# Kernel optimization log

Measured on AMD Instinct MI355X. Metric: run time of the kernel, lower is better.

Reference implementation:

```python
import math
import jax, jax.numpy as jnp
import numpy as np

D = 1024      # d_model
FF = 4096     # d_ff
E = 8         # num_experts
K = 2         # num_selected (top-k)
R = 2         # lora_rank (hardcoded in ToyMoEClassifier)
ALPHA = 4.0   # lora_alpha (hardcoded)
SCALE = ALPHA / R
CF = 1.25     # capacity_factor
NCLS = 2      # head output classes


def setup_inputs() -> dict:
    key = jax.random.key(0)
    ks = jax.random.split(key, 11)
    B, S = 4, 2048
    x = jax.random.normal(ks[0], (B, S, D), jnp.float32)
    Wg = jax.random.normal(ks[1], (D, E), jnp.float32) * 0.02
    W1 = jax.random.normal(ks[2], (D, FF), jnp.float32) * 0.02
    W2 = jax.random.normal(ks[3], (FF, D), jnp.float32) * 0.02
    A1 = jax.random.normal(ks[4], (E, D, R), jnp.float32) * 0.02
    B1 = jax.random.normal(ks[5], (E, R, FF), jnp.float32) * 0.02
    A2 = jax.random.normal(ks[6], (E, FF, R), jnp.float32) * 0.02
    B2 = jax.random.normal(ks[7], (E, R, D), jnp.float32) * 0.02
    Wh = jax.random.normal(ks[8], (D, NCLS), jnp.float32) * 0.02
    bh = jnp.zeros((NCLS,), jnp.float32)
    return {"x": x, "Wg": Wg, "W1": W1, "W2": W2, "A1": A1, "B1": B1,
            "A2": A2, "B2": B2, "Wh": Wh, "bh": bh}


def _moe_lora(x, Wg, W1, W2, A1, B1, A2, B2):
    B, S, d = x.shape
    T = B * S
    tok = x.reshape(T, d)                                  # [T, d]
    logits = tok @ Wg                                      # [T, E]
    vals, idx = jax.lax.top_k(logits, K)                   # [T, K]
    gates = jax.nn.softmax(vals, axis=-1)                  # renormalize over selected

    C = int(math.ceil(CF * T * K / E))                     # expert capacity (static)

    # position within expert, slot-major priority (slot 0 tokens first)
    onehot = jax.nn.one_hot(idx, E, dtype=jnp.float32)     # [T, K, E]
    m = onehot.transpose(1, 0, 2).reshape(K * T, E)        # [K*T, E]
    pos = jnp.cumsum(m, axis=0) - m
    pos_in = jnp.sum(pos * m, axis=-1).astype(jnp.int32)   # [K*T]
    exp_flat = idx.T.reshape(K * T)                        # [K*T]
    keep = (pos_in < C)
    w = gates.T.reshape(K * T) * keep.astype(gates.dtype)  # combine weight
    slot_idx = exp_flat * C + jnp.minimum(pos_in, C - 1)   # flat [E*C] index

    # dispatch: scatter kept tokens into per-expert capacity buffers
    disp = jnp.zeros((E * C, d), tok.dtype)
    for s in range(K):  # K is tiny and static
        sl = slice(s * T, (s + 1) * T)
        disp = disp.at[slot_idx[sl]].add(tok * keep[sl][:, None].astype(tok.dtype))
    disp3 = disp.reshape(E, C, d)

    # per-expert LoRA FFN: base weights shared, low-rank adapters per expert
    h = jax.nn.gelu(jnp.einsum('ecd,df->ecf', disp3, W1)
                    + SCALE * jnp.einsum('ecr,erf->ecf',
                                         jnp.einsum('ecd,edr->ecr', disp3, A1), B1))
    y = (jnp.einsum('ecf,fd->ecd', h, W2)
         + SCALE * jnp.einsum('ecr,erd->ecd',
                              jnp.einsum('ecf,efr->ecr', h, A2), B2))
    y_flat = y.reshape(E * C, d)

    # combine: gather expert outputs back, weighted by gates (dropped tokens -> 0)
    out = jnp.zeros((T, d), x.dtype)
    for s in range(K):
        sl = slice(s * T, (s + 1) * T)
        out = out + y_flat[slot_idx[sl]] * w[sl][:, None]
    return out.reshape(B, S, d)


def reference(x, Wg, W1, W2, A1, B1, A2, B2, Wh, bh):
    out = _moe_lora(x, Wg, W1, W2, A1, B1, A2, B2)   # [B, S, D]
    pooled = out.mean(axis=1)                        # [B, D]
    return pooled @ Wh + bh                          # [B, NCLS]
```

## Files before the change

### kernel.cpp

```cpp
#include <hip/hip_runtime.h>
#include <hip/hip_bf16.h>
#include <cstdint>
#include <cstddef>

#define D_MODEL 1024
#define FF_DIM  4096
#define NEXP    8
#define TOK     8192
#define CAP     2560
#define ECAP    (NEXP*CAP)
#define LSCALE  2.0f
#define SA_BYTE 124
#define SB_BYTE 122

typedef __attribute__((ext_vector_type(8))) int   int32x8;
typedef __attribute__((ext_vector_type(4))) float f32x4;
typedef __attribute__((ext_vector_type(2))) float f32x2;

__device__ __forceinline__ void gload16(const void* g, void* l){
  __builtin_amdgcn_global_load_lds((const __attribute__((address_space(1))) void*)g,
                                   (__attribute__((address_space(3))) void*)l, 16, 0, 0);
}
__device__ __forceinline__ float gelu_tanh(float x){
  float u = 0.7978845608028654f * (x + 0.044715f * x * x * x);
  float e = __expf(2.0f * u);
  float t = 1.0f - 2.0f / (e + 1.0f);
  return 0.5f * x * (1.0f + t);
}

__global__ void qt_both(const float* __restrict__ W1, const float* __restrict__ W2,
                        uint8_t* __restrict__ W1q, uint8_t* __restrict__ W2q)
{
  __shared__ float tile[64][65];
  const float* src; uint8_t* dst; int srcld, dstld;
  if (blockIdx.z == 0){ src = W1; dst = W1q; srcld = FF_DIM; dstld = D_MODEL; }
  else                { src = W2; dst = W2q; srcld = D_MODEL; dstld = FF_DIM; }
  int a0 = blockIdx.x * 64;
  int b0 = blockIdx.y * 64;
  if (blockIdx.z == 1){ a0 = blockIdx.y * 64; b0 = blockIdx.x * 64; }
  int tid = threadIdx.x;
  int r  = tid >> 4;
  int c4 = (tid & 15) * 4;
#pragma unroll
  for (int i = 0; i < 4; i++){
    int al = r + i*16;
    float4 v = *(const float4*)(src + (size_t)(a0 + al) * srcld + b0 + c4);
    tile[al][c4+0] = v.x; tile[al][c4+1] = v.y; tile[al][c4+2] = v.z; tile[al][c4+3] = v.w;
  }
  __syncthreads();
#pragma unroll
  for (int i = 0; i < 4; i++){
    int bl = r + i*16;
    int b  = b0 + bl;
    int pk = __builtin_amdgcn_cvt_pk_fp8_f32(32.f*tile[c4+0][bl], 32.f*tile[c4+1][bl], 0, false);
    pk     = __builtin_amdgcn_cvt_pk_fp8_f32(32.f*tile[c4+2][bl], 32.f*tile[c4+3][bl], pk, true);
    *(int*)(dst + (size_t)b * dstld + a0 + c4) = pk;
  }
}

__global__ void gate_kernel(const float* __restrict__ x, const float* __restrict__ Wg,
                            int* __restrict__ exp_flat, float* __restrict__ g_flat,
                            float* __restrict__ pooled, float* __restrict__ wslot)
{
  int gid = blockIdx.x * 256 + threadIdx.x;
  if (gid < 4*D_MODEL) pooled[gid] = 0.f;
  else if (gid < 4*D_MODEL + ECAP) wslot[gid - 4*D_MODEL] = 0.f;
  int lane = threadIdx.x & 63;
  int wave = threadIdx.x >> 6;
  int t = blockIdx.x * 4 + wave;
  const float4* xv = (const float4*)(x + (size_t)t * D_MODEL);
  float acc[8];
#pragma unroll
  for (int e = 0; e < 8; e++) acc[e] = 0.f;
#pragma unroll
  for (int i = 0; i < 4; i++){
    int i4 = lane + i*64;
    float4 v = xv[i4];
#pragma unroll
    for (int k = 0; k < 4; k++){
      float xs = (&v.x)[k];
      const float4* wr = (const float4*)(Wg + (size_t)(i4*4 + k) * 8);
      float4 w0 = wr[0], w1 = wr[1];
      acc[0] += xs*w0.x; acc[1] += xs*w0.y; acc[2] += xs*w0.z; acc[3] += xs*w0.w;
      acc[4] += xs*w1.x; acc[5] += xs*w1.y; acc[6] += xs*w1.z; acc[7] += xs*w1.w;
    }
  }
#pragma unroll
  for (int off = 32; off > 0; off >>= 1){
#pragma unroll
    for (int e = 0; e < 8; e++) acc[e] += __shfl_down(acc[e], off);
  }
  if (lane == 0){
    float m0 = acc[0]; int e0 = 0;
#pragma unroll
    for (int e = 1; e < 8; e++) if (acc[e] > m0){ m0 = acc[e]; e0 = e; }
    float m1 = -3.4e38f; int e1 = 0;
#pragma unroll
    for (int e = 0; e < 8; e++) if (e != e0 && acc[e] > m1){ m1 = acc[e]; e1 = e; }
    float z = __expf(m1 - m0);
    float inv = 1.f / (1.f + z);
    exp_flat[t]       = e0;
    exp_flat[TOK + t] = e1;
    g_flat[t]         = inv;
    g_flat[TOK + t]   = z * inv;
  }
}

__global__ __launch_bounds__(1024) void route_all(const int* __restrict__ exp_flat,
                                                  const float* __restrict__ g_flat,
                                                  int* __restrict__ slotidx,
                                                  float* __restrict__ wcomb,
                                                  int* __restrict__ fillc)
{
  __shared__ uint8_t rnk[16384];
  __shared__ uint8_t eexp[16384];
  __shared__ int     cnt[256*8];
  __shared__ int     grpoff[64];
  int tid = threadIdx.x;
  int lane = tid & 63, wv = tid >> 6;
  unsigned long long ltmask = (1ull << lane) - 1ull;
  for (int c = wv; c < 256; c += 16){
    int j = c*64 + lane;
    int e = exp_flat[j];
    eexp[j] = (uint8_t)e;
    int r = 0, myc = 0;
#pragma unroll
    for (int q = 0; q < 8; q++){
      unsigned long long m = __ballot(e == q);
      if (e == q) r = __popcll(m & ltmask);
      if (lane == q) myc = __popcll(m);
    }
    rnk[j] = (uint8_t)r;
    if (lane < 8) cnt[c*8 + lane] = myc;
  }
  __syncthreads();
  if (wv == 0){
    int e = lane & 7, g = lane >> 3;
    int run = 0;
    for (int c = g*32; c < g*32 + 32; c++){
      int v = cnt[c*8 + e];
      cnt[c*8 + e] = run;
      run += v;
    }
    int offs = 0, tot = 0;
#pragma unroll
    for (int gg = 0; gg < 8; gg++){
      int v = __shfl(run, gg*8 + e);
      if (gg < g) offs += v;
      tot += v;
    }
    grpoff[lane] = offs;
    if (g == 0) fillc[e] = tot < CAP ? tot : CAP;
  }
  __syncthreads();
  for (int j = tid; j < 16384; j += 1024){
    int e = eexp[j];
    int c = j >> 6;
    int pos = cnt[c*8 + e] + grpoff[(c >> 5)*8 + e] + rnk[j];
    bool keep = pos < CAP;
    slotidx[j] = e*CAP + (keep ? pos : (CAP-1));
    wcomb[j]   = keep ? g_flat[j] : 0.f;
  }
}

__global__ void dispatch_kernel(const float* __restrict__ x, const int* __restrict__ slotidx,
                                const float* __restrict__ wcomb, uint8_t* __restrict__ dispA,
                                float* __restrict__ wslot, int* __restrict__ tbat,
                                const float* __restrict__ A1, float* __restrict__ U1)
{
  int j = blockIdx.x;
  float w = wcomb[j];
  if (w == 0.f) return;
  int t = j & (TOK - 1);
  int slot = slotidx[j];
  int e = slot / CAP;
  int i = threadIdx.x;
  const float4* src = (const float4*)(x + (size_t)t * D_MODEL);
  float4 a = src[2*i], b = src[2*i+1];
  int p0 = __builtin_amdgcn_cvt_pk_fp8_f32(8.f*a.x, 8.f*a.y, 0, false);
  p0     = __builtin_amdgcn_cvt_pk_fp8_f32(8.f*a.z, 8.f*a.w, p0, true);
  int p1 = __builtin_amdgcn_cvt_pk_fp8_f32(8.f*b.x, 8.f*b.y, 0, false);
  p1     = __builtin_amdgcn_cvt_pk_fp8_f32(8.f*b.z, 8.f*b.w, p1, true);
  int2 o; o.x = p0; o.y = p1;
  *(int2*)(dispA + (size_t)slot * D_MODEL + i*8) = o;
  const float2* Av = (const float2*)(A1 + (size_t)e * D_MODEL * 2);
  int d0 = i*8;
  float xs[8] = {a.x,a.y,a.z,a.w,b.x,b.y,b.z,b.w};
  float pa = 0.f, pb = 0.f;
#pragma unroll
  for (int k = 0; k < 8; k++){
    float2 w2 = Av[d0 + k];
    pa += xs[k]*w2.x; pb += xs[k]*w2.y;
  }
#pragma unroll
  for (int off = 32; off > 0; off >>= 1){
    pa += __shfl_down(pa, off);
    pb += __shfl_down(pb, off);
  }
  __shared__ float red[4];
  int lane = i & 63, wv = i >> 6;
  if (lane == 0){ red[wv*2] = pa; red[wv*2+1] = pb; }
  __syncthreads();
  if (i == 0){
    U1[slot*2+0] = red[0] + red[2];
    U1[slot*2+1] = red[1] + red[3];
    wslot[slot] = w; tbat[slot] = t >> 11;
  }
}

__global__ void lora_u(const uint8_t* __restrict__ X, const float* __restrict__ Aw,
                       float* __restrict__ U, int Kdim)
{
  int lane = threadIdx.x & 63;
  int wv   = threadIdx.x >> 6;
  int slot = blockIdx.x * 4 + wv;
  int e = slot / CAP;
  const int4*   row = (const int4*)(X + (size_t)slot * Kdim);
  const float2* Av  = (const float2*)(Aw + (size_t)e * Kdim * 2);
  float a0 = 0.f, a1 = 0.f;
  int n16 = Kdim >> 4;
  for (int i = lane; i < n16; i += 64){
    int4 v = row[i];
    int d = i * 16;
#pragma unroll
    for (int c = 0; c < 4; c++){
      int w = (&v.x)[c];
      f32x2 f01 = __builtin_amdgcn_cvt_pk_f32_fp8(w, false);
      f32x2 f23 = __builtin_amdgcn_cvt_pk_f32_fp8(w, true);
      int dd = d + c*4;
      float2 w0 = Av[dd], w1 = Av[dd+1], w2 = Av[dd+2], w3 = Av[dd+3];
      a0 += f01.x*w0.x + f01.y*w1.x + f23.x*w2.x + f23.y*w3.x;
      a1 += f01.x*w0.y + f01.y*w1.y + f23.x*w2.y + f23.y*w3.y;
    }
  }
#pragma unroll
  for (int off = 32; off > 0; off >>= 1){
    a0 += __shfl_down(a0, off);
    a1 += __shfl_down(a1, off);
  }
  if (lane == 0){ U[slot*2] = a0 * 0.125f; U[slot*2+1] = a1 * 0.125f; }
}

template<bool GELU, bool COMBINE>
__global__ __launch_bounds__(256) void gemm_mx(const uint8_t* __restrict__ A,
                                               const uint8_t* __restrict__ Bt,
                                               uint8_t* __restrict__ Cb,
                                               int K, int N, const int* __restrict__ fillc,
                                               const float* __restrict__ U,
                                               const float* __restrict__ Bl,
                                               const float* __restrict__ wslot,
                                               const int* __restrict__ tbat,
                                               float* __restrict__ pooled)
{
  int e = blockIdx.x / 20;
  if ((blockIdx.x % 20) * 128 >= fillc[e]) return;
  int row0 = blockIdx.x * 128;
  int col0 = blockIdx.y * 128;

  __shared__ __align__(16) uint8_t As[128*128];
  __shared__ __align__(16) uint8_t Bs[128*128];
  __shared__ float part[COMBINE ? 512 : 4];

  int tid  = threadIdx.x;
  int lane = tid & 63;
  int wave = tid >> 6;
  int wm = wave & 1, wn = wave >> 1;

  if (COMBINE){ part[tid] = 0.f; part[tid + 256] = 0.f; }

  int r8 = lane >> 3;
  int cs = (lane & 7) ^ r8;
  const uint8_t* gA = A  + (size_t)(row0 + wave*32 + r8) * K + cs*16;
  const uint8_t* gB = Bt + (size_t)(col0 + wave*32 + r8) * K + cs*16;
  uint8_t* lA = As + wave*32*128;
  uint8_t* lB = Bs + wave*32*128;

  int rb = lane & 15;
  int q  = lane >> 4;

  f32x4 acc[4][4];
#pragma unroll
  for (int i = 0; i < 4; i++)
#pragma unroll
    for (int j = 0; j < 4; j++)
      acc[i][j] = (f32x4){0.f, 0.f, 0.f, 0.f};

  for (int k0 = 0; k0 < K; k0 += 128){
    __syncthreads();
#pragma unroll
    for (int g = 0; g < 4; g++){
      gload16(gA + k0 + (size_t)g*8*K, lA + g*1024);
      gload16(gB + k0 + (size_t)g*8*K, lB + g*1024);
    }
    __syncthreads();
    int32x8 a[4], b[4];
#pragma unroll
    for (int mt = 0; mt < 4; mt++){
      int row = wm*64 + mt*16 + rb;
      const uint8_t* base = As + row*128;
      int sw = row & 7;
      int4 lo = *(const int4*)(base + (((2*q)  ^sw)*16));
      int4 hi = *(const int4*)(base + (((2*q+1)^sw)*16));
      int32x8 v; v[0]=lo.x; v[1]=lo.y; v[2]=lo.z; v[3]=lo.w;
                 v[4]=hi.x; v[5]=hi.y; v[6]=hi.z; v[7]=hi.w;
      a[mt] = v;
    }
#pragma unroll
    for (int nt = 0; nt < 4; nt++){
      int row = wn*64 + nt*16 + rb;
      const uint8_t* base = Bs + row*128;
      int sw = row & 7;
      int4 lo = *(const int4*)(base + (((2*q)  ^sw)*16));
      int4 hi = *(const int4*)(base + (((2*q+1)^sw)*16));
      int32x8 v; v[0]=lo.x; v[1]=lo.y; v[2]=lo.z; v[3]=lo.w;
                 v[4]=hi.x; v[5]=hi.y; v[6]=hi.z; v[7]=hi.w;
      b[nt] = v;
    }
#pragma unroll
    for (int mt = 0; mt < 4; mt++)
#pragma unroll
      for (int nt = 0; nt < 4; nt++)
        acc[mt][nt] = __builtin_amdgcn_mfma_scale_f32_16x16x128_f8f6f4(
            a[mt], b[nt], acc[mt][nt], 0, 0, 0, SA_BYTE, 0, SB_BYTE);
  }

  float b0c[4], b1c[4];
#pragma unroll
  for (int nt = 0; nt < 4; nt++){
    int col = col0 + wn*64 + rb + nt*16;
    b0c[nt] = Bl[(e*2+0)*N + col];
    b1c[nt] = Bl[(e*2+1)*N + col];
  }

#pragma unroll
  for (int mt = 0; mt < 4; mt++){
#pragma unroll
    for (int r = 0; r < 4; r++){
      int row = row0 + wm*64 + mt*16 + q*4 + r;
      float2 u = *(const float2*)(U + row*2);
      float wv = 0.f; int tb = 0;
      if (COMBINE){ wv = wslot[row]; tb = tbat[row]; }
      size_t base = (size_t)row * N + col0 + wn*64 + rb;
#pragma unroll
      for (int nt = 0; nt < 4; nt++){
        float v = acc[mt][nt][r] + LSCALE*(u.x*b0c[nt] + u.y*b1c[nt]);
        if (GELU){
          v = gelu_tanh(v);
          int pk = __builtin_amdgcn_cvt_pk_fp8_f32(8.f*v, 0.f, 0, false);
          Cb[base + nt*16] = (uint8_t)(pk & 0xFF);
        }
        if (COMBINE){
          if (wv != 0.f) atomicAdd(&part[tb*128 + wn*64 + rb + nt*16], wv*v);
        }
      }
    }
  }

  if (COMBINE){
    __syncthreads();
#pragma unroll
    for (int idx = tid; idx < 512; idx += 256){
      float pv = part[idx];
      if (pv != 0.f) atomicAdd(pooled + (size_t)(idx >> 7) * D_MODEL + col0 + (idx & 127), pv);
    }
  }
}

__global__ void head_kernel(const float* __restrict__ pooled, const float* __restrict__ Wh,
                            const float* __restrict__ bh, float* __restrict__ out)
{
  int lane = threadIdx.x & 63;
  int wave = threadIdx.x >> 6;
  int b = wave >> 1, c = wave & 1;
  float s = 0.f;
#pragma unroll
  for (int i = 0; i < 16; i++){
    int d = lane + i*64;
    s += pooled[(size_t)b * D_MODEL + d] * Wh[d*2 + c];
  }
#pragma unroll
  for (int off = 32; off > 0; off >>= 1) s += __shfl_down(s, off);
  if (lane == 0) out[b*2 + c] = s * (1.0f/2048.0f) + bh[c];
}

extern "C" void kernel_launch(void* const* d_in, const int* in_sizes, int n_in,
                              void* d_out, int out_size, void* d_ws, size_t ws_size,
                              hipStream_t stream)
{
  const float* x  = (const float*)d_in[0];
  const float* Wg = (const float*)d_in[1];
  const float* W1 = (const float*)d_in[2];
  const float* W2 = (const float*)d_in[3];
  const float* A1 = (const float*)d_in[4];
  const float* B1 = (const float*)d_in[5];
  const float* A2 = (const float*)d_in[6];
  const float* B2 = (const float*)d_in[7];
  const float* Wh = (const float*)d_in[8];
  const float* bh = (const float*)d_in[9];
  float* out = (float*)d_out;

  char* p = (char*)d_ws;
  auto alloc = [&](size_t bytes){
    char* r = p;
    p += (bytes + 255) & ~(size_t)255;
    return (void*)r;
  };
  uint8_t* W1q   = (uint8_t*)alloc((size_t)FF_DIM*D_MODEL);
  uint8_t* W2q   = (uint8_t*)alloc((size_t)D_MODEL*FF_DIM);
  uint8_t* dispA = (uint8_t*)alloc((size_t)ECAP*D_MODEL);
  uint8_t* H     = (uint8_t*)alloc((size_t)ECAP*FF_DIM);
  float* U1       = (float*)alloc((size_t)ECAP*2*4);
  float* U2       = (float*)alloc((size_t)ECAP*2*4);
  float* wslot    = (float*)alloc((size_t)ECAP*4);
  int*   tbat     = (int*)  alloc((size_t)ECAP*4);
  int*   exp_flat = (int*)  alloc((size_t)2*TOK*4);
  float* g_flat   = (float*)alloc((size_t)2*TOK*4);
  int*   slotidx  = (int*)  alloc((size_t)2*TOK*4);
  float* wcomb    = (float*)alloc((size_t)2*TOK*4);
  int*   fillc    = (int*)  alloc(256);
  float* pooled   = (float*)alloc((size_t)4*D_MODEL*4);

  qt_both<<<dim3(16,64,2), 256, 0, stream>>>(W1, W2, W1q, W2q);
  gate_kernel<<<2048, 256, 0, stream>>>(x, Wg, exp_flat, g_flat, pooled, wslot);
  route_all<<<1, 1024, 0, stream>>>(exp_flat, g_flat, slotidx, wcomb, fillc);
  dispatch_kernel<<<2*TOK, 128, 0, stream>>>(x, slotidx, wcomb, dispA, wslot, tbat, A1, U1);
  gemm_mx<true, false><<<dim3(160,32), 256, 0, stream>>>(dispA, W1q, H, D_MODEL, FF_DIM,
                                                         fillc, U1, B1, nullptr, nullptr, nullptr);
  lora_u<<<5120, 256, 0, stream>>>(H, A2, U2, FF_DIM);
  gemm_mx<false, true><<<dim3(160,8), 256, 0, stream>>>(H, W2q, nullptr, FF_DIM, D_MODEL,
                                                        fillc, U2, B2, wslot, tbat, pooled);
  head_kernel<<<1, 512, 0, stream>>>(pooled, Wh, bh, out);
}
```

Before: 580.5 us.

## Halve GEMM M-tile to 64 rows and fuse gate with weight quantization

The fp8 MFMA GEMMs now use 64x128 tiles instead of 128x128. This doubles the grid, reduces skipped-tile waste at expert fill boundaries, and with launch_bounds(256,4) allows higher occupancy. The cost is less reuse of the B tile per loaded A row. The gating and weight-quantization kernels are merged into one launch so their blocks run concurrently and one launch is saved.

```diff
diff --git a/kernel.cpp b/kernel.cpp
--- a/kernel.cpp
+++ b/kernel.cpp
@@ -28,81 +28,82 @@
   return 0.5f * x * (1.0f + t);
 }
 
-__global__ void qt_both(const float* __restrict__ W1, const float* __restrict__ W2,
-                        uint8_t* __restrict__ W1q, uint8_t* __restrict__ W2q)
+__global__ void prep_kernel(const float* __restrict__ x, const float* __restrict__ Wg,
+                            int* __restrict__ exp_flat, float* __restrict__ g_flat,
+                            float* __restrict__ pooled, float* __restrict__ wslot,
+                            const float* __restrict__ W1, const float* __restrict__ W2,
+                            uint8_t* __restrict__ W1q, uint8_t* __restrict__ W2q)
 {
   __shared__ float tile[64][65];
-  const float* src; uint8_t* dst; int srcld, dstld;
-  if (blockIdx.z == 0){ src = W1; dst = W1q; srcld = FF_DIM; dstld = D_MODEL; }
-  else                { src = W2; dst = W2q; srcld = D_MODEL; dstld = FF_DIM; }
-  int a0 = blockIdx.x * 64;
-  int b0 = blockIdx.y * 64;
-  if (blockIdx.z == 1){ a0 = blockIdx.y * 64; b0 = blockIdx.x * 64; }
+  int bx = blockIdx.x;
   int tid = threadIdx.x;
-  int r  = tid >> 4;
-  int c4 = (tid & 15) * 4;
-#pragma unroll
-  for (int i = 0; i < 4; i++){
-    int al = r + i*16;
-    float4 v = *(const float4*)(src + (size_t)(a0 + al) * srcld + b0 + c4);
-    tile[al][c4+0] = v.x; tile[al][c4+1] = v.y; tile[al][c4+2] = v.z; tile[al][c4+3] = v.w;
-  }
-  __syncthreads();
-#pragma unroll
-  for (int i = 0; i < 4; i++){
-    int bl = r + i*16;
-    int b  = b0 + bl;
-    int pk = __builtin_amdgcn_cvt_pk_fp8_f32(32.f*tile[c4+0][bl], 32.f*tile[c4+1][bl], 0, false);
-    pk     = __builtin_amdgcn_cvt_pk_fp8_f32(32.f*tile[c4+2][bl], 32.f*tile[c4+3][bl], pk, true);
-    *(int*)(dst + (size_t)b * dstld + a0 + c4) = pk;
-  }
-}
-
-__global__ void gate_kernel(const float* __restrict__ x, const float* __restrict__ Wg,
-                            int* __restrict__ exp_flat, float* __restrict__ g_flat,
-                            float* __restrict__ pooled, float* __restrict__ wslot)
-{
-  int gid = blockIdx.x * 256 + threadIdx.x;
-  if (gid < 4*D_MODEL) pooled[gid] = 0.f;
-  else if (gid < 4*D_MODEL + ECAP) wslot[gid - 4*D_MODEL] = 0.f;
-  int lane = threadIdx.x & 63;
-  int wave = threadIdx.x >> 6;
-  int t = blockIdx.x * 4 + wave;
-  const float4* xv = (const float4*)(x + (size_t)t * D_MODEL);
-  float acc[8];
-#pragma unroll
-  for (int e = 0; e < 8; e++) acc[e] = 0.f;
-#pragma unroll
-  for (int i = 0; i < 4; i++){
-    int i4 = lane + i*64;
-    float4 v = xv[i4];
-#pragma unroll
-    for (int k = 0; k < 4; k++){
-      float xs = (&v.x)[k];
-      const float4* wr = (const float4*)(Wg + (size_t)(i4*4 + k) * 8);
-      float4 w0 = wr[0], w1 = wr[1];
-      acc[0] += xs*w0.x; acc[1] += xs*w0.y; acc[2] += xs*w0.z; acc[3] += xs*w0.w;
-      acc[4] += xs*w1.x; acc[5] += xs*w1.y; acc[6] += xs*w1.z; acc[7] += xs*w1.w;
-    }
-  }
-#pragma unroll
-  for (int off = 32; off > 0; off >>= 1){
-#pragma unroll
-    for (int e = 0; e < 8; e++) acc[e] += __shfl_down(acc[e], off);
-  }
-  if (lane == 0){
-    float m0 = acc[0]; int e0 = 0;
-#pragma unroll
-    for (int e = 1; e < 8; e++) if (acc[e] > m0){ m0 = acc[e]; e0 = e; }
-    float m1 = -3.4e38f; int e1 = 0;
-#pragma unroll
-    for (int e = 0; e < 8; e++) if (e != e0 && acc[e] > m1){ m1 = acc[e]; e1 = e; }
-    float z = __expf(m1 - m0);
-    float inv = 1.f / (1.f + z);
-    exp_flat[t]       = e0;
-    exp_flat[TOK + t] = e1;
-    g_flat[t]         = inv;
-    g_flat[TOK + t]   = z * inv;
+  if (bx < 2048){
+    int gid = bx * 256 + tid;
+    if (gid < 4*D_MODEL) pooled[gid] = 0.f;
+    else if (gid < 4*D_MODEL + ECAP) wslot[gid - 4*D_MODEL] = 0.f;
+    int lane = tid & 63;
+    int wave = tid >> 6;
+    int t = bx * 4 + wave;
+    const float4* xv = (const float4*)(x + (size_t)t * D_MODEL);
+    float acc[8];
+#pragma unroll
+    for (int e = 0; e < 8; e++) acc[e] = 0.f;
+#pragma unroll
+    for (int i = 0; i < 4; i++){
+      int i4 = lane + i*64;
+      float4 v = xv[i4];
+#pragma unroll
+      for (int k = 0; k < 4; k++){
+        float xs = (&v.x)[k];
+        const float4* wr = (const float4*)(Wg + (size_t)(i4*4 + k) * 8);
+        float4 w0 = wr[0], w1 = wr[1];
+        acc[0] += xs*w0.x; acc[1] += xs*w0.y; acc[2] += xs*w0.z; acc[3] += xs*w0.w;
+        acc[4] += xs*w1.x; acc[5] += xs*w1.y; acc[6] += xs*w1.z; acc[7] += xs*w1.w;
+      }
+    }
+#pragma unroll
+    for (int off = 32; off > 0; off >>= 1){
+#pragma unroll
+      for (int e = 0; e < 8; e++) acc[e] += __shfl_down(acc[e], off);
+    }
+    if (lane == 0){
+      float m0 = acc[0]; int e0 = 0;
+#pragma unroll
+      for (int e = 1; e < 8; e++) if (acc[e] > m0){ m0 = acc[e]; e0 = e; }
+      float m1 = -3.4e38f; int e1 = 0;
+#pragma unroll
+      for (int e = 0; e < 8; e++) if (e != e0 && acc[e] > m1){ m1 = acc[e]; e1 = e; }
+      float z = __expf(m1 - m0);
+      float inv = 1.f / (1.f + z);
+      exp_flat[t]       = e0;
+      exp_flat[TOK + t] = e1;
+      g_flat[t]         = inv;
+      g_flat[TOK + t]   = z * inv;
+    }
+  } else {
+    int b = bx - 2048;
+    int z = b >> 10; b &= 1023;
+    int bxx = b & 15, byy = b >> 4;
+    const float* src; uint8_t* dst; int srcld, dstld, a0, b0;
+    if (z == 0){ src = W1; dst = W1q; srcld = FF_DIM; dstld = D_MODEL; a0 = bxx*64; b0 = byy*64; }
+    else       { src = W2; dst = W2q; srcld = D_MODEL; dstld = FF_DIM; a0 = byy*64; b0 = bxx*64; }
+    int r  = tid >> 4;
+    int c4 = (tid & 15) * 4;
+#pragma unroll
+    for (int i = 0; i < 4; i++){
+      int al = r + i*16;
+      float4 v = *(const float4*)(src + (size_t)(a0 + al) * srcld + b0 + c4);
+      tile[al][c4+0] = v.x; tile[al][c4+1] = v.y; tile[al][c4+2] = v.z; tile[al][c4+3] = v.w;
+    }
+    __syncthreads();
+#pragma unroll
+    for (int i = 0; i < 4; i++){
+      int bl = r + i*16;
+      int bb = b0 + bl;
+      int pk = __builtin_amdgcn_cvt_pk_fp8_f32(32.f*tile[c4+0][bl], 32.f*tile[c4+1][bl], 0, false);
+      pk     = __builtin_amdgcn_cvt_pk_fp8_f32(32.f*tile[c4+2][bl], 32.f*tile[c4+3][bl], pk, true);
+      *(int*)(dst + (size_t)bb * dstld + a0 + c4) = pk;
+    }
   }
 }
 
@@ -242,22 +243,22 @@
 }
 
 template<bool GELU, bool COMBINE>
-__global__ __launch_bounds__(256) void gemm_mx(const uint8_t* __restrict__ A,
-                                               const uint8_t* __restrict__ Bt,
-                                               uint8_t* __restrict__ Cb,
-                                               int K, int N, const int* __restrict__ fillc,
-                                               const float* __restrict__ U,
-                                               const float* __restrict__ Bl,
-                                               const float* __restrict__ wslot,
-                                               const int* __restrict__ tbat,
-                                               float* __restrict__ pooled)
-{
-  int e = blockIdx.x / 20;
-  if ((blockIdx.x % 20) * 128 >= fillc[e]) return;
-  int row0 = blockIdx.x * 128;
+__global__ __launch_bounds__(256, 4) void gemm_mx(const uint8_t* __restrict__ A,
+                                                  const uint8_t* __restrict__ Bt,
+                                                  uint8_t* __restrict__ Cb,
+                                                  int K, int N, const int* __restrict__ fillc,
+                                                  const float* __restrict__ U,
+                                                  const float* __restrict__ Bl,
+                                                  const float* __restrict__ wslot,
+                                                  const int* __restrict__ tbat,
+                                                  float* __restrict__ pooled)
+{
+  int e = blockIdx.x / 40;
+  if ((blockIdx.x % 40) * 64 >= fillc[e]) return;
+  int row0 = blockIdx.x * 64;
   int col0 = blockIdx.y * 128;
 
-  __shared__ __align__(16) uint8_t As[128*128];
+  __shared__ __align__(16) uint8_t As[64*128];
   __shared__ __align__(16) uint8_t Bs[128*128];
   __shared__ float part[COMBINE ? 512 : 4];
 
@@ -270,17 +271,17 @@
 
   int r8 = lane >> 3;
   int cs = (lane & 7) ^ r8;
-  const uint8_t* gA = A  + (size_t)(row0 + wave*32 + r8) * K + cs*16;
+  const uint8_t* gA = A  + (size_t)(row0 + wave*16 + r8) * K + cs*16;
   const uint8_t* gB = Bt + (size_t)(col0 + wave*32 + r8) * K + cs*16;
-  uint8_t* lA = As + wave*32*128;
+  uint8_t* lA = As + wave*16*128;
   uint8_t* lB = Bs + wave*32*128;
 
   int rb = lane & 15;
   int q  = lane >> 4;
 
-  f32x4 acc[4][4];
-#pragma unroll
-  for (int i = 0; i < 4; i++)
+  f32x4 acc[2][4];
+#pragma unroll
+  for (int i = 0; i < 2; i++)
 #pragma unroll
     for (int j = 0; j < 4; j++)
       acc[i][j] = (f32x4){0.f, 0.f, 0.f, 0.f};
@@ -288,15 +289,16 @@
   for (int k0 = 0; k0 < K; k0 += 128){
     __syncthreads();
 #pragma unroll
-    for (int g = 0; g < 4; g++){
+    for (int g = 0; g < 2; g++)
       gload16(gA + k0 + (size_t)g*8*K, lA + g*1024);
+#pragma unroll
+    for (int g = 0; g < 4; g++)
       gload16(gB + k0 + (size_t)g*8*K, lB + g*1024);
-    }
     __syncthreads();
-    int32x8 a[4], b[4];
-#pragma unroll
-    for (int mt = 0; mt < 4; mt++){
-      int row = wm*64 + mt*16 + rb;
+    int32x8 a[2], b[4];
+#pragma unroll
+    for (int mt = 0; mt < 2; mt++){
+      int row = wm*32 + mt*16 + rb;
       const uint8_t* base = As + row*128;
       int sw = row & 7;
       int4 lo = *(const int4*)(base + (((2*q)  ^sw)*16));
@@ -317,7 +319,7 @@
       b[nt] = v;
     }
 #pragma unroll
-    for (int mt = 0; mt < 4; mt++)
+    for (int mt = 0; mt < 2; mt++)
 #pragma unroll
       for (int nt = 0; nt < 4; nt++)
         acc[mt][nt] = __builtin_amdgcn_mfma_scale_f32_16x16x128_f8f6f4(
@@ -333,10 +335,10 @@
   }
 
 #pragma unroll
-  for (int mt = 0; mt < 4; mt++){
+  for (int mt = 0; mt < 2; mt++){
 #pragma unroll
     for (int r = 0; r < 4; r++){
-      int row = row0 + wm*64 + mt*16 + q*4 + r;
+      int row = row0 + wm*32 + mt*16 + q*4 + r;
       float2 u = *(const float2*)(U + row*2);
       float wv = 0.f; int tb = 0;
       if (COMBINE){ wv = wslot[row]; tb = tbat[row]; }
@@ -420,14 +422,14 @@
   int*   fillc    = (int*)  alloc(256);
   float* pooled   = (float*)alloc((size_t)4*D_MODEL*4);
 
-  qt_both<<<dim3(16,64,2), 256, 0, stream>>>(W1, W2, W1q, W2q);
-  gate_kernel<<<2048, 256, 0, stream>>>(x, Wg, exp_flat, g_flat, pooled, wslot);
+  prep_kernel<<<4096, 256, 0, stream>>>(x, Wg, exp_flat, g_flat, pooled, wslot,
+                                        W1, W2, W1q, W2q);
   route_all<<<1, 1024, 0, stream>>>(exp_flat, g_flat, slotidx, wcomb, fillc);
   dispatch_kernel<<<2*TOK, 128, 0, stream>>>(x, slotidx, wcomb, dispA, wslot, tbat, A1, U1);
-  gemm_mx<true, false><<<dim3(160,32), 256, 0, stream>>>(dispA, W1q, H, D_MODEL, FF_DIM,
+  gemm_mx<true, false><<<dim3(320,32), 256, 0, stream>>>(dispA, W1q, H, D_MODEL, FF_DIM,
                                                          fillc, U1, B1, nullptr, nullptr, nullptr);
   lora_u<<<5120, 256, 0, stream>>>(H, A2, U2, FF_DIM);
-  gemm_mx<false, true><<<dim3(160,8), 256, 0, stream>>>(H, W2q, nullptr, FF_DIM, D_MODEL,
+  gemm_mx<false, true><<<dim3(320,8), 256, 0, stream>>>(H, W2q, nullptr, FF_DIM, D_MODEL,
                                                         fillc, U2, B2, wslot, tbat, pooled);
   head_kernel<<<1, 512, 0, stream>>>(pooled, Wh, bh, out);
 }
```

After: 579.7 us. Within noise of the previous version (-0.1%).

## Collapse second expert GEMM by pooling gated hidden activations before W2

Applied to the files above, without the earlier changes.

Mean pooling and the W2/LoRA projection are linear, so the code first sums the gate-weighted FP8 hidden activations per batch and expert (ge_reduce). It then applies A2/B2 and the fp32 W2 once per batch vector (collapse, final_pool). This removes the full second expert GEMM, the lora_u pass and the W2 FP8 quantization. W1 quantization is merged into the gate kernel launch. The cost is a serial reduction over H with atomics and a small fp32 GEMV against W2, and summation order and precision change slightly.

```diff
diff --git a/kernel.cpp b/kernel.cpp
--- a/kernel.cpp
+++ b/kernel.cpp
@@ -28,81 +28,80 @@
   return 0.5f * x * (1.0f + t);
 }
 
-__global__ void qt_both(const float* __restrict__ W1, const float* __restrict__ W2,
-                        uint8_t* __restrict__ W1q, uint8_t* __restrict__ W2q)
+__global__ void prep_kernel(const float* __restrict__ x, const float* __restrict__ Wg,
+                            int* __restrict__ exp_flat, float* __restrict__ g_flat,
+                            float* __restrict__ pooled, float* __restrict__ wslot,
+                            float* __restrict__ Ge,
+                            const float* __restrict__ W1, uint8_t* __restrict__ W1q)
 {
   __shared__ float tile[64][65];
-  const float* src; uint8_t* dst; int srcld, dstld;
-  if (blockIdx.z == 0){ src = W1; dst = W1q; srcld = FF_DIM; dstld = D_MODEL; }
-  else                { src = W2; dst = W2q; srcld = D_MODEL; dstld = FF_DIM; }
-  int a0 = blockIdx.x * 64;
-  int b0 = blockIdx.y * 64;
-  if (blockIdx.z == 1){ a0 = blockIdx.y * 64; b0 = blockIdx.x * 64; }
+  int bx = blockIdx.x;
   int tid = threadIdx.x;
-  int r  = tid >> 4;
-  int c4 = (tid & 15) * 4;
-#pragma unroll
-  for (int i = 0; i < 4; i++){
-    int al = r + i*16;
-    float4 v = *(const float4*)(src + (size_t)(a0 + al) * srcld + b0 + c4);
-    tile[al][c4+0] = v.x; tile[al][c4+1] = v.y; tile[al][c4+2] = v.z; tile[al][c4+3] = v.w;
-  }
-  __syncthreads();
-#pragma unroll
-  for (int i = 0; i < 4; i++){
-    int bl = r + i*16;
-    int b  = b0 + bl;
-    int pk = __builtin_amdgcn_cvt_pk_fp8_f32(32.f*tile[c4+0][bl], 32.f*tile[c4+1][bl], 0, false);
-    pk     = __builtin_amdgcn_cvt_pk_fp8_f32(32.f*tile[c4+2][bl], 32.f*tile[c4+3][bl], pk, true);
-    *(int*)(dst + (size_t)b * dstld + a0 + c4) = pk;
-  }
-}
-
-__global__ void gate_kernel(const float* __restrict__ x, const float* __restrict__ Wg,
-                            int* __restrict__ exp_flat, float* __restrict__ g_flat,
-                            float* __restrict__ pooled, float* __restrict__ wslot)
-{
-  int gid = blockIdx.x * 256 + threadIdx.x;
-  if (gid < 4*D_MODEL) pooled[gid] = 0.f;
-  else if (gid < 4*D_MODEL + ECAP) wslot[gid - 4*D_MODEL] = 0.f;
-  int lane = threadIdx.x & 63;
-  int wave = threadIdx.x >> 6;
-  int t = blockIdx.x * 4 + wave;
-  const float4* xv = (const float4*)(x + (size_t)t * D_MODEL);
-  float acc[8];
-#pragma unroll
-  for (int e = 0; e < 8; e++) acc[e] = 0.f;
-#pragma unroll
-  for (int i = 0; i < 4; i++){
-    int i4 = lane + i*64;
-    float4 v = xv[i4];
-#pragma unroll
-    for (int k = 0; k < 4; k++){
-      float xs = (&v.x)[k];
-      const float4* wr = (const float4*)(Wg + (size_t)(i4*4 + k) * 8);
-      float4 w0 = wr[0], w1 = wr[1];
-      acc[0] += xs*w0.x; acc[1] += xs*w0.y; acc[2] += xs*w0.z; acc[3] += xs*w0.w;
-      acc[4] += xs*w1.x; acc[5] += xs*w1.y; acc[6] += xs*w1.z; acc[7] += xs*w1.w;
-    }
-  }
-#pragma unroll
-  for (int off = 32; off > 0; off >>= 1){
-#pragma unroll
-    for (int e = 0; e < 8; e++) acc[e] += __shfl_down(acc[e], off);
-  }
-  if (lane == 0){
-    float m0 = acc[0]; int e0 = 0;
-#pragma unroll
-    for (int e = 1; e < 8; e++) if (acc[e] > m0){ m0 = acc[e]; e0 = e; }
-    float m1 = -3.4e38f; int e1 = 0;
-#pragma unroll
-    for (int e = 0; e < 8; e++) if (e != e0 && acc[e] > m1){ m1 = acc[e]; e1 = e; }
-    float z = __expf(m1 - m0);
-    float inv = 1.f / (1.f + z);
-    exp_flat[t]       = e0;
-    exp_flat[TOK + t] = e1;
-    g_flat[t]         = inv;
-    g_flat[TOK + t]   = z * inv;
+  if (bx < 2048){
+    int gid = bx * 256 + tid;
+    if (gid < 4*D_MODEL) pooled[gid] = 0.f;
+    else if (gid < 4*D_MODEL + ECAP) wslot[gid - 4*D_MODEL] = 0.f;
+    else if (gid < 4*D_MODEL + ECAP + 4*NEXP*FF_DIM) Ge[gid - 4*D_MODEL - ECAP] = 0.f;
+    int lane = tid & 63;
+    int wave = tid >> 6;
+    int t = bx * 4 + wave;
+    const float4* xv = (const float4*)(x + (size_t)t * D_MODEL);
+    float acc[8];
+#pragma unroll
+    for (int e = 0; e < 8; e++) acc[e] = 0.f;
+#pragma unroll
+    for (int i = 0; i < 4; i++){
+      int i4 = lane + i*64;
+      float4 v = xv[i4];
+#pragma unroll
+      for (int k = 0; k < 4; k++){
+        float xs = (&v.x)[k];
+        const float4* wr = (const float4*)(Wg + (size_t)(i4*4 + k) * 8);
+        float4 w0 = wr[0], w1 = wr[1];
+        acc[0] += xs*w0.x; acc[1] += xs*w0.y; acc[2] += xs*w0.z; acc[3] += xs*w0.w;
+        acc[4] += xs*w1.x; acc[5] += xs*w1.y; acc[6] += xs*w1.z; acc[7] += xs*w1.w;
+      }
+    }
+#pragma unroll
+    for (int off = 32; off > 0; off >>= 1){
+#pragma unroll
+      for (int e = 0; e < 8; e++) acc[e] += __shfl_down(acc[e], off);
+    }
+    if (lane == 0){
+      float m0 = acc[0]; int e0 = 0;
+#pragma unroll
+      for (int e = 1; e < 8; e++) if (acc[e] > m0){ m0 = acc[e]; e0 = e; }
+      float m1 = -3.4e38f; int e1 = 0;
+#pragma unroll
+      for (int e = 0; e < 8; e++) if (e != e0 && acc[e] > m1){ m1 = acc[e]; e1 = e; }
+      float z = __expf(m1 - m0);
+      float inv = 1.f / (1.f + z);
+      exp_flat[t]       = e0;
+      exp_flat[TOK + t] = e1;
+      g_flat[t]         = inv;
+      g_flat[TOK + t]   = z * inv;
+    }
+  } else {
+    int b = bx - 2048;
+    int d0 = (b & 15) * 64;
+    int f0 = (b >> 4) * 64;
+    int r  = tid >> 4;
+    int c4 = (tid & 15) * 4;
+#pragma unroll
+    for (int i = 0; i < 4; i++){
+      int dl = r + i*16;
+      float4 v = *(const float4*)(W1 + (size_t)(d0 + dl) * FF_DIM + f0 + c4);
+      tile[dl][c4+0] = v.x; tile[dl][c4+1] = v.y; tile[dl][c4+2] = v.z; tile[dl][c4+3] = v.w;
+    }
+    __syncthreads();
+#pragma unroll
+    for (int i = 0; i < 4; i++){
+      int fl = r + i*16;
+      int f  = f0 + fl;
+      int pk = __builtin_amdgcn_cvt_pk_fp8_f32(32.f*tile[c4+0][fl], 32.f*tile[c4+1][fl], 0, false);
+      pk     = __builtin_amdgcn_cvt_pk_fp8_f32(32.f*tile[c4+2][fl], 32.f*tile[c4+3][fl], pk, true);
+      *(int*)(W1q + (size_t)f * D_MODEL + d0 + c4) = pk;
+    }
   }
 }
 
@@ -208,49 +207,12 @@
   }
 }
 
-__global__ void lora_u(const uint8_t* __restrict__ X, const float* __restrict__ Aw,
-                       float* __restrict__ U, int Kdim)
-{
-  int lane = threadIdx.x & 63;
-  int wv   = threadIdx.x >> 6;
-  int slot = blockIdx.x * 4 + wv;
-  int e = slot / CAP;
-  const int4*   row = (const int4*)(X + (size_t)slot * Kdim);
-  const float2* Av  = (const float2*)(Aw + (size_t)e * Kdim * 2);
-  float a0 = 0.f, a1 = 0.f;
-  int n16 = Kdim >> 4;
-  for (int i = lane; i < n16; i += 64){
-    int4 v = row[i];
-    int d = i * 16;
-#pragma unroll
-    for (int c = 0; c < 4; c++){
-      int w = (&v.x)[c];
-      f32x2 f01 = __builtin_amdgcn_cvt_pk_f32_fp8(w, false);
-      f32x2 f23 = __builtin_amdgcn_cvt_pk_f32_fp8(w, true);
-      int dd = d + c*4;
-      float2 w0 = Av[dd], w1 = Av[dd+1], w2 = Av[dd+2], w3 = Av[dd+3];
-      a0 += f01.x*w0.x + f01.y*w1.x + f23.x*w2.x + f23.y*w3.x;
-      a1 += f01.x*w0.y + f01.y*w1.y + f23.x*w2.y + f23.y*w3.y;
-    }
-  }
-#pragma unroll
-  for (int off = 32; off > 0; off >>= 1){
-    a0 += __shfl_down(a0, off);
-    a1 += __shfl_down(a1, off);
-  }
-  if (lane == 0){ U[slot*2] = a0 * 0.125f; U[slot*2+1] = a1 * 0.125f; }
-}
-
-template<bool GELU, bool COMBINE>
 __global__ __launch_bounds__(256) void gemm_mx(const uint8_t* __restrict__ A,
                                                const uint8_t* __restrict__ Bt,
                                                uint8_t* __restrict__ Cb,
                                                int K, int N, const int* __restrict__ fillc,
                                                const float* __restrict__ U,
-                                               const float* __restrict__ Bl,
-                                               const float* __restrict__ wslot,
-                                               const int* __restrict__ tbat,
-                                               float* __restrict__ pooled)
+                                               const float* __restrict__ Bl)
 {
   int e = blockIdx.x / 20;
   if ((blockIdx.x % 20) * 128 >= fillc[e]) return;
@@ -259,14 +221,11 @@
 
   __shared__ __align__(16) uint8_t As[128*128];
   __shared__ __align__(16) uint8_t Bs[128*128];
-  __shared__ float part[COMBINE ? 512 : 4];
 
   int tid  = threadIdx.x;
   int lane = tid & 63;
   int wave = tid >> 6;
   int wm = wave & 1, wn = wave >> 1;
-
-  if (COMBINE){ part[tid] = 0.f; part[tid + 256] = 0.f; }
 
   int r8 = lane >> 3;
   int cs = (lane & 7) ^ r8;
@@ -338,32 +297,117 @@
     for (int r = 0; r < 4; r++){
       int row = row0 + wm*64 + mt*16 + q*4 + r;
       float2 u = *(const float2*)(U + row*2);
-      float wv = 0.f; int tb = 0;
-      if (COMBINE){ wv = wslot[row]; tb = tbat[row]; }
       size_t base = (size_t)row * N + col0 + wn*64 + rb;
 #pragma unroll
       for (int nt = 0; nt < 4; nt++){
         float v = acc[mt][nt][r] + LSCALE*(u.x*b0c[nt] + u.y*b1c[nt]);
-        if (GELU){
-          v = gelu_tanh(v);
-          int pk = __builtin_amdgcn_cvt_pk_fp8_f32(8.f*v, 0.f, 0, false);
-          Cb[base + nt*16] = (uint8_t)(pk & 0xFF);
-        }
-        if (COMBINE){
-          if (wv != 0.f) atomicAdd(&part[tb*128 + wn*64 + rb + nt*16], wv*v);
-        }
+        v = gelu_tanh(v);
+        int pk = __builtin_amdgcn_cvt_pk_fp8_f32(8.f*v, 0.f, 0, false);
+        Cb[base + nt*16] = (uint8_t)(pk & 0xFF);
       }
     }
   }
-
-  if (COMBINE){
+}
+
+__global__ void ge_reduce(const uint8_t* __restrict__ H, const float* __restrict__ wslot,
+                          const int* __restrict__ tbat, float* __restrict__ Ge)
+{
+  int sc = blockIdx.x;
+  int f0 = blockIdx.y * 512;
+  int e  = sc / 20;
+  int tid = threadIdx.x;
+  __shared__ float wsl[128];
+  __shared__ int   tbl[128];
+  if (tid < 128){
+    int slot = sc*128 + tid;
+    wsl[tid] = wslot[slot] * 0.125f;
+    tbl[tid] = tbat[slot];
+  }
+  __syncthreads();
+  float2 a0 = {0,0}, a1 = {0,0}, a2 = {0,0}, a3 = {0,0};
+  const uint8_t* hp = H + (size_t)sc*128*FF_DIM + f0 + tid*2;
+  for (int s = 0; s < 128; s++){
+    float w = wsl[s];
+    if (w != 0.f){
+      int tb = tbl[s];
+      unsigned short raw = *(const unsigned short*)(hp + (size_t)s*FF_DIM);
+      f32x2 hv = __builtin_amdgcn_cvt_pk_f32_fp8((int)raw, false);
+      float h0 = w*hv.x, h1 = w*hv.y;
+      if      (tb == 0){ a0.x += h0; a0.y += h1; }
+      else if (tb == 1){ a1.x += h0; a1.y += h1; }
+      else if (tb == 2){ a2.x += h0; a2.y += h1; }
+      else             { a3.x += h0; a3.y += h1; }
+    }
+  }
+  int f = f0 + tid*2;
+  atomicAdd(&Ge[((0*8+e)*FF_DIM) + f],   a0.x); atomicAdd(&Ge[((0*8+e)*FF_DIM) + f+1], a0.y);
+  atomicAdd(&Ge[((1*8+e)*FF_DIM) + f],   a1.x); atomicAdd(&Ge[((1*8+e)*FF_DIM) + f+1], a1.y);
+  atomicAdd(&Ge[((2*8+e)*FF_DIM) + f],   a2.x); atomicAdd(&Ge[((2*8+e)*FF_DIM) + f+1], a2.y);
+  atomicAdd(&Ge[((3*8+e)*FF_DIM) + f],   a3.x); atomicAdd(&Ge[((3*8+e)*FF_DIM) + f+1], a3.y);
+}
+
+__global__ void collapse(const float* __restrict__ Ge, const float* __restrict__ A2,
+                         float* __restrict__ G, float* __restrict__ P)
+{
+  int bx = blockIdx.x, tid = threadIdx.x;
+  if (bx < 32){
+    int b = bx >> 3, e = bx & 7;
+    const float*  g  = Ge + (size_t)(b*8+e)*FF_DIM;
+    const float2* Av = (const float2*)(A2 + (size_t)e*FF_DIM*2);
+    float p0 = 0.f, p1 = 0.f;
+    for (int f = tid; f < FF_DIM; f += 256){
+      float gv = g[f];
+      float2 a = Av[f];
+      p0 += gv*a.x; p1 += gv*a.y;
+    }
+#pragma unroll
+    for (int off = 32; off > 0; off >>= 1){
+      p0 += __shfl_down(p0, off);
+      p1 += __shfl_down(p1, off);
+    }
+    __shared__ float red[8];
+    int lane = tid & 63, wv = tid >> 6;
+    if (lane == 0){ red[wv*2] = p0; red[wv*2+1] = p1; }
     __syncthreads();
-#pragma unroll
-    for (int idx = tid; idx < 512; idx += 256){
-      float pv = part[idx];
-      if (pv != 0.f) atomicAdd(pooled + (size_t)(idx >> 7) * D_MODEL + col0 + (idx & 127), pv);
-    }
-  }
+    if (tid == 0){
+      P[(b*8+e)*2+0] = red[0]+red[2]+red[4]+red[6];
+      P[(b*8+e)*2+1] = red[1]+red[3]+red[5]+red[7];
+    }
+  } else {
+    for (int c = (bx-32)*1024 + tid; c < (bx-31)*1024; c += 256){
+      int b = c >> 12, f = c & 4095;
+      float s = 0.f;
+#pragma unroll
+      for (int e = 0; e < 8; e++) s += Ge[(size_t)(b*8+e)*FF_DIM + f];
+      G[b*FF_DIM + f] = s;
+    }
+  }
+}
+
+__global__ void final_pool(const float* __restrict__ G, const float* __restrict__ W2,
+                           const float* __restrict__ P, const float* __restrict__ B2,
+                           float* __restrict__ pooled)
+{
+  int bx = blockIdx.x, tid = threadIdx.x;
+  int b  = bx >> 4;
+  int r  = bx & 15;
+  int fq = r >> 2, db = r & 3;
+  int d  = db*256 + tid;
+  const float* g = G  + (size_t)b*FF_DIM + fq*1024;
+  const float* w = W2 + (size_t)fq*1024*D_MODEL + d;
+  float acc = 0.f;
+#pragma unroll 4
+  for (int f = 0; f < 1024; f++) acc += g[f] * w[(size_t)f*D_MODEL];
+  if (fq == 0){
+    float lt = 0.f;
+#pragma unroll
+    for (int e = 0; e < 8; e++){
+      lt += P[(b*8+e)*2+0]*B2[(e*2+0)*D_MODEL + d]
+          + P[(b*8+e)*2+1]*B2[(e*2+1)*D_MODEL + d];
+    }
+    acc += LSCALE*lt;
+  }
+  atomicAdd(&pooled[b*D_MODEL + d], acc);
 }
 
 __global__ void head_kernel(const float* __restrict__ pooled, const float* __restrict__ Wh,
@@ -406,11 +450,9 @@
     return (void*)r;
   };
   uint8_t* W1q   = (uint8_t*)alloc((size_t)FF_DIM*D_MODEL);
-  uint8_t* W2q   = (uint8_t*)alloc((size_t)D_MODEL*FF_DIM);
   uint8_t* dispA = (uint8_t*)alloc((size_t)ECAP*D_MODEL);
   uint8_t* H     = (uint8_t*)alloc((size_t)ECAP*FF_DIM);
   float* U1       = (float*)alloc((size_t)ECAP*2*4);
-  float* U2       = (float*)alloc((size_t)ECAP*2*4);
   float* wslot    = (float*)alloc((size_t)ECAP*4);
   int*   tbat     = (int*)  alloc((size_t)ECAP*4);
   int*   exp_flat = (int*)  alloc((size_t)2*TOK*4);
@@ -419,15 +461,16 @@
   float* wcomb    = (float*)alloc((size_t)2*TOK*4);
   int*   fillc    = (int*)  alloc(256);
   float* pooled   = (float*)alloc((size_t)4*D_MODEL*4);
-
-  qt_both<<<dim3(16,64,2), 256, 0, stream>>>(W1, W2, W1q, W2q);
-  gate_kernel<<<2048, 256, 0, stream>>>(x, Wg, exp_flat, g_flat, pooled, wslot);
+  float* Ge       = (float*)alloc((size_t)4*NEXP*FF_DIM*4);
+  float* G        = (float*)alloc((size_t)4*FF_DIM*4);
+  float* P        = (float*)alloc((size_t)4*NEXP*2*4);
+
+  prep_kernel<<<3072, 256, 0, stream>>>(x, Wg, exp_flat, g_flat, pooled, wslot, Ge, W1, W1q);
   route_all<<<1, 1024, 0, stream>>>(exp_flat, g_flat, slotidx, wcomb, fillc);
   dispatch_kernel<<<2*TOK, 128, 0, stream>>>(x, slotidx, wcomb, dispA, wslot, tbat, A1, U1);
-  gemm_mx<true, false><<<dim3(160,32), 256, 0, stream>>>(dispA, W1q, H, D_MODEL, FF_DIM,
-                                                         fillc, U1, B1, nullptr, nullptr, nullptr);
-  lora_u<<<5120, 256, 0, stream>>>(H, A2, U2, FF_DIM);
-  gemm_mx<false, true><<<dim3(160,8), 256, 0, stream>>>(H, W2q, nullptr, FF_DIM, D_MODEL,
-                                                        fillc, U2, B2, wslot, tbat, pooled);
+  gemm_mx<<<dim3(160,32), 256, 0, stream>>>(dispA, W1q, H, D_MODEL, FF_DIM, fillc, U1, B1);
+  ge_reduce<<<dim3(160,8), 256, 0, stream>>>(H, wslot, tbat, Ge);
+  collapse<<<48, 256, 0, stream>>>(Ge, A2, G, P);
+  final_pool<<<64, 256, 0, stream>>>(G, W2, P, B2, pooled);
   head_kernel<<<1, 512, 0, stream>>>(pooled, Wh, bh, out);
 }
```

After: 507.7 us. 12.5% less time.
